# Optimization experiments

Hardware: AMD Instinct MI355X
Metric: run time of the kernel (lower is better)

Reference implementation:

```python
import jax, jax.numpy as jnp
import numpy as np

L, B, H, E, V = 64, 2048, 512, 50, 96
PAD = 0  # padding_idx of the char embedding


def setup_inputs() -> dict:
    key = jax.random.key(0)
    ks = jax.random.split(key, 10)
    s = 0.1  # param scale to keep gates in a sane range
    emb = jax.random.normal(ks[0], (V, E), jnp.float32) * s
    emb = emb.at[PAD].set(0.0)  # padding_idx row is zero
    return {
        "input_ids": jax.random.randint(ks[1], (L, B), 0, V),
        "h0": jax.random.normal(ks[2], (1, B, H), jnp.float32) * s,
        "c0": jax.random.normal(ks[3], (1, B, H), jnp.float32) * s,
        "emb": emb,
        "W_ih": jax.random.normal(ks[4], (4 * H, E), jnp.float32) * s,
        "W_hh": jax.random.normal(ks[5], (4 * H, H), jnp.float32) * s,
        "b_ih": jax.random.normal(ks[6], (4 * H,), jnp.float32) * s,
        "b_hh": jax.random.normal(ks[7], (4 * H,), jnp.float32) * s,
        "W_out": jax.random.normal(ks[8], (V, H), jnp.float32) * s,
        "b_out": jax.random.normal(ks[9], (V,), jnp.float32) * s,
    }


def reference(input_ids, h0, c0, emb, W_ih, W_hh, b_ih, b_hh, W_out, b_out):
    # Embedding lookup: (L, B, E)
    x = emb[input_ids]
    # Precompute input-side gate contributions for all steps: (L, B, 4H)
    x_gates = jnp.einsum('lbe,ge->lbg', x, W_ih) + b_ih + b_hh

    def step(carry, xg):
        h, c = carry  # (B, H) each
        gates = xg + h @ W_hh.T  # (B, 4H), PyTorch gate order i, f, g, o
        i, f, g, o = jnp.split(gates, 4, axis=-1)
        c_new = jax.nn.sigmoid(f) * c + jax.nn.sigmoid(i) * jnp.tanh(g)
        h_new = jax.nn.sigmoid(o) * jnp.tanh(c_new)
        return (h_new, c_new), h_new

    (hL, cL), hs = jax.lax.scan(step, (h0[0], c0[0]), x_gates)
    # Output projection on every step's hidden state: (L, B, V)
    scores = jnp.einsum('lbh,vh->lbv', hs, W_out) + b_out
    return scores, hL[None], cL[None]
```

## Files before the change

kernel.cpp:

```cpp
#include <hip/hip_runtime.h>
#include <stdint.h>

#define LSEQ 64
#define BATCH 2048
#define HID 512
#define NG 2048
#define KP 576
#define VOCAB 96
#define BH (BATCH*HID)

#define WLDS_OFF 0
#define RING_OFF 98304
#define HPK_OFF  147456
#define SMEM_TOT 155648

typedef unsigned short u16;
typedef __attribute__((ext_vector_type(8))) short short8;
typedef __attribute__((ext_vector_type(4))) float f32x4;

__device__ __forceinline__ u16 f2bf(float f) {
    union { float f; unsigned u; } v; v.f = f;
    return (u16)((v.u + 0x7FFFu + ((v.u >> 16) & 1u)) >> 16);
}
__device__ __forceinline__ float sig_(float x) { return 1.f / (1.f + __expf(-x)); }
__device__ __forceinline__ float th_(float x) {
    x = fminf(fmaxf(x, -30.f), 30.f);
    float e = __expf(2.f * x);
    return (e - 1.f) / (e + 1.f);
}
__device__ __forceinline__ void gld16(const void* g, void* l) {
    __builtin_amdgcn_global_load_lds(
        (const __attribute__((address_space(1))) unsigned int*)g,
        (__attribute__((address_space(3))) unsigned int*)l, 16, 0, 0);
}
#define WAITV(n) asm volatile("s_waitcnt vmcnt(" #n ")" ::: "memory")

__global__ void k_init(const float* __restrict__ h0, u16* __restrict__ hs0,
                       unsigned* __restrict__ flags) {
    int i = blockIdx.x * 256 + threadIdx.x;
    hs0[i] = f2bf(h0[i]);
    if (i < LSEQ * 256) flags[i] = 0;
}

__global__ void k_pack_w(const float* __restrict__ Wih, const float* __restrict__ Whh,
                         const float* __restrict__ bih, const float* __restrict__ bhh,
                         u16* __restrict__ Wp, float* __restrict__ bp) {
    int id = blockIdx.x * 256 + threadIdx.x;
    int n = id / 72, kc = id % 72;
    int j = n >> 2, q = n & 3;
    int src = q * HID + j;
    int k0 = kc * 8;
    unsigned pk[4];
#pragma unroll
    for (int t = 0; t < 4; ++t) {
        int k = k0 + 2 * t;
        float f0 = (k < 512) ? Whh[src * 512 + k] : ((k < 562) ? Wih[src * 50 + k - 512] : 0.f);
        float f1 = (k + 1 < 512) ? Whh[src * 512 + k + 1]
                                 : ((k + 1 < 562) ? Wih[src * 50 + k + 1 - 512] : 0.f);
        pk[t] = (unsigned)f2bf(f0) | ((unsigned)f2bf(f1) << 16);
    }
    *(uint4*)(Wp + (size_t)n * KP + k0) = make_uint4(pk[0], pk[1], pk[2], pk[3]);
    if (kc == 0) bp[n] = bih[src] + bhh[src];
}

__global__ void k_embed(const int* __restrict__ ids, const float* __restrict__ emb,
                        u16* __restrict__ xb) {
    int id = blockIdx.x * 256 + threadIdx.x;
    int row = id >> 3, kc = id & 7;
    int tok = ids[row];
    int k0 = kc * 8;
    unsigned pk[4];
#pragma unroll
    for (int t = 0; t < 4; ++t) {
        int k = k0 + 2 * t;
        unsigned lo = (k < 50) ? (unsigned)f2bf(emb[tok * 50 + k]) : 0u;
        unsigned hi = (k + 1 < 50) ? (unsigned)f2bf(emb[tok * 50 + k + 1]) : 0u;
        pk[t] = lo | (hi << 16);
    }
    *(uint4*)(xb + (size_t)row * 64 + k0) = make_uint4(pk[0], pk[1], pk[2], pk[3]);
}

__global__ void k_pack_wout(const float* __restrict__ Wo, u16* __restrict__ Wb) {
    int id = blockIdx.x * 256 + threadIdx.x;
    int k0 = id * 8;
    unsigned pk[4];
#pragma unroll
    for (int t = 0; t < 4; ++t)
        pk[t] = (unsigned)f2bf(Wo[k0 + 2 * t]) | ((unsigned)f2bf(Wo[k0 + 2 * t + 1]) << 16);
    *(uint4*)(Wb + k0) = make_uint4(pk[0], pk[1], pk[2], pk[3]);
}

__global__ __launch_bounds__(256, 1) void k_persist(
    const u16* __restrict__ xb, const u16* __restrict__ Wp,
    const float* __restrict__ bp, const float* __restrict__ c0,
    u16* __restrict__ hs, float* __restrict__ foutH, float* __restrict__ foutC,
    unsigned* __restrict__ flags)
{
    extern __shared__ char smem[];
    char* Wlds = smem + WLDS_OFF;
    char* ring = smem + RING_OFF;
    u16*  hpk  = (u16*)(smem + HPK_OFF);

    const int tid = threadIdx.x;
    const int lane = tid & 63;
    const int w = tid >> 6;
    const int wm = w >> 1, wn = w & 1;
    const int bm = blockIdx.x & 15, bn = blockIdx.x >> 4;
    const int m0 = bm * 128, n0 = bn * 128;
    const int rsub = lane >> 3;
    const int colsw = (((lane & 7) ^ rsub) << 3);
    const int bsub = lane & 15;
    const int usub = lane >> 4;

#pragma unroll
    for (int t = 0; t < 6; ++t)
#pragma unroll
        for (int it = 0; it < 4; ++it) {
            int wc = w * 4 + it;
            gld16(Wp + (size_t)(n0 + wc * 8 + rsub) * KP + (t + 2) * 64 + colsw,
                  Wlds + t * 16384 + wc * 1024);
        }

    short8 wreg[3][2][4];
#pragma unroll
    for (int t = 0; t < 3; ++t) {
        const int koff = (t == 0) ? 512 : (t - 1) * 64;
#pragma unroll
        for (int kk = 0; kk < 2; ++kk)
#pragma unroll
            for (int qm = 0; qm < 4; ++qm)
                wreg[t][kk][qm] = *(const short8*)(
                    Wp + (size_t)(n0 + wm * 64 + qm * 16 + bsub) * KP
                       + koff + kk * 32 + usub * 8);
    }

    float4 bb[4];
#pragma unroll
    for (int qm = 0; qm < 4; ++qm)
        bb[qm] = *(const float4*)(bp + n0 + wm * 64 + qm * 16 + usub * 4);
    float c[4][4];
#pragma unroll
    for (int qm = 0; qm < 4; ++qm)
#pragma unroll
        for (int qn = 0; qn < 4; ++qn)
            c[qm][qn] = c0[(size_t)(m0 + wn * 64 + qn * 16 + bsub) * HID
                           + (n0 >> 2) + wm * 16 + qm * 4 + usub];

    WAITV(0);
    __syncthreads();

#pragma unroll 1
    for (int l = 0; l < LSEQ; ++l) {
        const u16* hsrc = hs + (size_t)l * BH;

        {
            const u16* xs = xb + (size_t)l * BATCH * 64;
#pragma unroll
            for (int it = 0; it < 4; ++it) {
                int wc = w * 4 + it;
                gld16(xs + (size_t)(m0 + wc * 8 + rsub) * 64 + colsw, ring + wc * 1024);
            }
        }
        if (l > 0 && w == 0) {
            const unsigned* f = flags + (unsigned)(l - 1) * 256 + bm * 16;
            for (;;) {
                unsigned v = (lane < 16)
                    ? __hip_atomic_load(f + lane, __ATOMIC_RELAXED, __HIP_MEMORY_SCOPE_AGENT)
                    : 1u;
                if (__all(v != 0)) break;
                __builtin_amdgcn_s_sleep(2);
            }
        }
        __syncthreads();
        __builtin_amdgcn_sched_barrier(0);

#pragma unroll
        for (int it = 0; it < 4; ++it) {
            int wc = w * 4 + it;
            gld16(hsrc + (size_t)(m0 + wc * 8 + rsub) * HID + colsw,
                  ring + 16384 + wc * 1024);
        }

        f32x4 acc[4][4] = {};
#pragma unroll
        for (int i = 0; i < 9; ++i) {
            if (i > 0) {
                if (i < 8) WAITV(4); else WAITV(0);
                __builtin_amdgcn_s_barrier();
                __builtin_amdgcn_sched_barrier(0);
            }
            if (i + 2 <= 8) {
                char* dst = ring + ((i + 2) % 3) * 16384;
#pragma unroll
                for (int it = 0; it < 4; ++it) {
                    int wc = w * 4 + it;
                    gld16(hsrc + (size_t)(m0 + wc * 8 + rsub) * HID + (i + 1) * 64 + colsw,
                          dst + wc * 1024);
                }
            }
            const u16* Bs_ = (const u16*)(ring + (i % 3) * 16384);
#pragma unroll
            for (int kk = 0; kk < 2; ++kk) {
                short8 hv[4];
#pragma unroll
                for (int qn = 0; qn < 4; ++qn)
                    hv[qn] = *(const short8*)(Bs_ + (wn * 64 + qn * 16 + bsub) * 64
                                 + (((kk * 4 + usub) ^ (lane & 7)) << 3));
                short8 wf[4];
                if (i <= 2) {
#pragma unroll
                    for (int qm = 0; qm < 4; ++qm) wf[qm] = wreg[i][kk][qm];
                } else {
                    const u16* Ws_ = (const u16*)(Wlds + (i - 3) * 16384);
#pragma unroll
                    for (int qm = 0; qm < 4; ++qm)
                        wf[qm] = *(const short8*)(Ws_ + (wm * 64 + qm * 16 + bsub) * 64
                                     + (((kk * 4 + usub) ^ (lane & 7)) << 3));
                }
#pragma unroll
                for (int qm = 0; qm < 4; ++qm)
#pragma unroll
                    for (int qn = 0; qn < 4; ++qn)
                        acc[qm][qn] = __builtin_amdgcn_mfma_f32_16x16x32_bf16(
                            wf[qm], hv[qn], acc[qm][qn], 0, 0, 0);
            }
        }

        const bool last = (l == LSEQ - 1);
#pragma unroll
        for (int qm = 0; qm < 4; ++qm) {
            const float4 b4 = bb[qm];
            const int u_loc = wm * 16 + qm * 4 + usub;
#pragma unroll
            for (int qn = 0; qn < 4; ++qn) {
                const int b_loc = wn * 64 + qn * 16 + bsub;
                float gi = acc[qm][qn][0] + b4.x;
                float gf = acc[qm][qn][1] + b4.y;
                float gg = acc[qm][qn][2] + b4.z;
                float go = acc[qm][qn][3] + b4.w;
                float cn = sig_(gf) * c[qm][qn] + sig_(gi) * th_(gg);
                float hn = sig_(go) * th_(cn);
                c[qm][qn] = cn;
                hpk[b_loc * 32 + (u_loc ^ ((b_loc & 7) << 2))] = f2bf(hn);
                if (last) {
                    size_t ci = (size_t)(m0 + b_loc) * HID + (n0 >> 2) + u_loc;
                    foutH[ci] = hn; foutC[ci] = cn;
                }
            }
        }
        __syncthreads();

        {
            const int b = tid >> 1, hf = tid & 1;
            unsigned long long q[4];
#pragma unroll
            for (int g = 0; g < 4; ++g) {
                int G = hf * 4 + g;
                int gs = G ^ (b & 7);
                q[g] = *(const unsigned long long*)((const char*)hpk + b * 64 + gs * 8);
            }
            u16* dst = hs + (size_t)(l + 1) * BH + (size_t)(m0 + b) * HID
                       + (n0 >> 2) + hf * 16;
            *(uint4*)(dst)     = make_uint4((unsigned)q[0], (unsigned)(q[0] >> 32),
                                            (unsigned)q[1], (unsigned)(q[1] >> 32));
            *(uint4*)(dst + 8) = make_uint4((unsigned)q[2], (unsigned)(q[2] >> 32),
                                            (unsigned)q[3], (unsigned)(q[3] >> 32));
        }
        WAITV(0);
        __syncthreads();
        if (tid == 0)
            __hip_atomic_store(flags + (unsigned)l * 256 + bm * 16 + bn, 1u,
                               __ATOMIC_RELAXED, __HIP_MEMORY_SCOPE_AGENT);
    }
}

__global__ __launch_bounds__(256) void k_scores(
    const u16* __restrict__ hsall, const u16* __restrict__ Wb,
    const float* __restrict__ bo, float* __restrict__ out)
{
    __shared__ char smem[28672];
    u16* As = (u16*)smem;
    u16* Bs = (u16*)(smem + 16384);
    const int tid = threadIdx.x, lane = tid & 63, w = tid >> 6;
    const size_t m0 = (size_t)blockIdx.x * 128;
    const int colo = (lane & 7) * 8;
    const int rsub = lane >> 3;
    f32x4 acc[2][6] = {};

    for (int kt = 0; kt < 8; ++kt) {
#pragma unroll
        for (int it = 0; it < 4; ++it) {
            int wc = w * 4 + it;
            int r = wc * 8 + rsub;
            gld16(hsall + (m0 + r) * 512 + kt * 64 + colo, smem + wc * 1024);
        }
#pragma unroll
        for (int it = 0; it < 3; ++it) {
            int wc = w * 3 + it;
            int r = wc * 8 + rsub;
            gld16(Wb + (size_t)r * 512 + kt * 64 + colo, smem + 16384 + wc * 1024);
        }
        __syncthreads();
#pragma unroll
        for (int kk = 0; kk < 2; ++kk) {
            short8 av[2], bv[6];
#pragma unroll
            for (int i = 0; i < 2; ++i)
                av[i] = *(const short8*)(As + (w * 32 + i * 16 + (lane & 15)) * 64 + kk * 32 + (lane >> 4) * 8);
#pragma unroll
            for (int j = 0; j < 6; ++j)
                bv[j] = *(const short8*)(Bs + (j * 16 + (lane & 15)) * 64 + kk * 32 + (lane >> 4) * 8);
#pragma unroll
            for (int i = 0; i < 2; ++i)
#pragma unroll
                for (int j = 0; j < 6; ++j)
                    acc[i][j] = __builtin_amdgcn_mfma_f32_16x16x32_bf16(av[i], bv[j], acc[i][j], 0, 0, 0);
        }
        __syncthreads();
    }
#pragma unroll
    for (int i = 0; i < 2; ++i) {
        int ml = w * 32 + i * 16 + (lane >> 4) * 4;
#pragma unroll
        for (int j = 0; j < 6; ++j) {
            int v = j * 16 + (lane & 15);
            float bbv = bo[v];
#pragma unroll
            for (int r = 0; r < 4; ++r)
                out[(m0 + ml + r) * 96 + v] = acc[i][j][r] + bbv;
        }
    }
}

extern "C" void kernel_launch(void* const* d_in, const int* in_sizes, int n_in,
                              void* d_out, int out_size, void* d_ws, size_t ws_size,
                              hipStream_t stream) {
    const int*   ids  = (const int*)d_in[0];
    const float* h0   = (const float*)d_in[1];
    const float* c0   = (const float*)d_in[2];
    const float* emb  = (const float*)d_in[3];
    const float* Wih  = (const float*)d_in[4];
    const float* Whh  = (const float*)d_in[5];
    const float* bih  = (const float*)d_in[6];
    const float* bhh  = (const float*)d_in[7];
    const float* Wout = (const float*)d_in[8];
    const float* bout = (const float*)d_in[9];

    char* ws = (char*)d_ws;
    u16*      hs    = (u16*)ws;
    unsigned* flags = (unsigned*)(ws + 136314880);
    u16*      xb    = (u16*)(ws + 140509184);
    u16*      Wp    = (u16*)(ws + 157286400);
    float*    bp    = (float*)(ws + 159645696);
    u16*      Wb    = (u16*)(ws + 159653888);
    float*    out   = (float*)d_out;

    k_init<<<dim3(BH / 256), dim3(256), 0, stream>>>(h0, hs, flags);
    k_pack_w<<<dim3(NG * 72 / 256), dim3(256), 0, stream>>>(Wih, Whh, bih, bhh, Wp, bp);
    k_embed<<<dim3(LSEQ * BATCH * 8 / 256), dim3(256), 0, stream>>>(ids, emb, xb);
    k_pack_wout<<<dim3(VOCAB * HID / 8 / 256), dim3(256), 0, stream>>>(Wout, Wb);

    hipFuncSetAttribute((const void*)k_persist,
                        hipFuncAttributeMaxDynamicSharedMemorySize, SMEM_TOT);
    k_persist<<<dim3(256), dim3(256), SMEM_TOT, stream>>>(
        xb, Wp, bp, c0, hs, out + 12582912, out + 12582912 + BH, flags);

    k_scores<<<dim3(LSEQ * BATCH / 128), dim3(256), 0, stream>>>(hs + BH, Wb, bout, out);
}
```

Before: 577.2 us.

## Load h and x operands directly into registers, keep all W_hh slices in LDS

```diff
diff --git a/kernel.cpp b/kernel.cpp
--- a/kernel.cpp
+++ b/kernel.cpp
@@ -10,9 +10,8 @@
 #define BH (BATCH*HID)
 
 #define WLDS_OFF 0
-#define RING_OFF 98304
-#define HPK_OFF  147456
-#define SMEM_TOT 155648
+#define HPK_OFF  131072
+#define SMEM_TOT 139264
 
 typedef unsigned short u16;
 typedef __attribute__((ext_vector_type(8))) short short8;
@@ -98,7 +97,6 @@
 {
     extern __shared__ char smem[];
     char* Wlds = smem + WLDS_OFF;
-    char* ring = smem + RING_OFF;
     u16*  hpk  = (u16*)(smem + HPK_OFF);
 
     const int tid = threadIdx.x;
@@ -111,28 +109,25 @@
     const int colsw = (((lane & 7) ^ rsub) << 3);
     const int bsub = lane & 15;
     const int usub = lane >> 4;
-
-#pragma unroll
-    for (int t = 0; t < 6; ++t)
+    const int brow = m0 + wn * 64 + bsub;
+
+#pragma unroll
+    for (int t = 0; t < 8; ++t)
 #pragma unroll
         for (int it = 0; it < 4; ++it) {
             int wc = w * 4 + it;
-            gld16(Wp + (size_t)(n0 + wc * 8 + rsub) * KP + (t + 2) * 64 + colsw,
+            gld16(Wp + (size_t)(n0 + wc * 8 + rsub) * KP + t * 64 + colsw,
                   Wlds + t * 16384 + wc * 1024);
         }
 
-    short8 wreg[3][2][4];
-#pragma unroll
-    for (int t = 0; t < 3; ++t) {
-        const int koff = (t == 0) ? 512 : (t - 1) * 64;
-#pragma unroll
-        for (int kk = 0; kk < 2; ++kk)
-#pragma unroll
-            for (int qm = 0; qm < 4; ++qm)
-                wreg[t][kk][qm] = *(const short8*)(
-                    Wp + (size_t)(n0 + wm * 64 + qm * 16 + bsub) * KP
-                       + koff + kk * 32 + usub * 8);
-    }
+    short8 wrx[2][4];
+#pragma unroll
+    for (int kk = 0; kk < 2; ++kk)
+#pragma unroll
+        for (int qm = 0; qm < 4; ++qm)
+            wrx[kk][qm] = *(const short8*)(
+                Wp + (size_t)(n0 + wm * 64 + qm * 16 + bsub) * KP
+                   + 512 + kk * 32 + usub * 8);
 
     float4 bb[4];
 #pragma unroll
@@ -143,24 +138,26 @@
     for (int qm = 0; qm < 4; ++qm)
 #pragma unroll
         for (int qn = 0; qn < 4; ++qn)
-            c[qm][qn] = c0[(size_t)(m0 + wn * 64 + qn * 16 + bsub) * HID
+            c[qm][qn] = c0[(size_t)(brow + qn * 16) * HID
                            + (n0 >> 2) + wm * 16 + qm * 4 + usub];
 
     WAITV(0);
     __syncthreads();
+
+    short8 pA[8], pB[8];
 
 #pragma unroll 1
     for (int l = 0; l < LSEQ; ++l) {
         const u16* hsrc = hs + (size_t)l * BH;
-
-        {
-            const u16* xs = xb + (size_t)l * BATCH * 64;
-#pragma unroll
-            for (int it = 0; it < 4; ++it) {
-                int wc = w * 4 + it;
-                gld16(xs + (size_t)(m0 + wc * 8 + rsub) * 64 + colsw, ring + wc * 1024);
-            }
-        }
+        const u16* xsrc = xb + (size_t)l * BATCH * 64;
+
+#pragma unroll
+        for (int kk = 0; kk < 2; ++kk)
+#pragma unroll
+            for (int qn = 0; qn < 4; ++qn)
+                pA[kk * 4 + qn] = *(const short8*)(
+                    xsrc + (size_t)(brow + qn * 16) * 64 + kk * 32 + usub * 8);
+
         if (l > 0 && w == 0) {
             const unsigned* f = flags + (unsigned)(l - 1) * 256 + bm * 16;
             for (;;) {
@@ -175,43 +172,26 @@
         __builtin_amdgcn_sched_barrier(0);
 
 #pragma unroll
-        for (int it = 0; it < 4; ++it) {
-            int wc = w * 4 + it;
-            gld16(hsrc + (size_t)(m0 + wc * 8 + rsub) * HID + colsw,
-                  ring + 16384 + wc * 1024);
-        }
+        for (int kk = 0; kk < 2; ++kk)
+#pragma unroll
+            for (int qn = 0; qn < 4; ++qn)
+                pB[kk * 4 + qn] = *(const short8*)(
+                    hsrc + (size_t)(brow + qn * 16) * HID + kk * 32 + usub * 8);
 
         f32x4 acc[4][4] = {};
 #pragma unroll
         for (int i = 0; i < 9; ++i) {
-            if (i > 0) {
-                if (i < 8) WAITV(4); else WAITV(0);
-                __builtin_amdgcn_s_barrier();
-                __builtin_amdgcn_sched_barrier(0);
-            }
-            if (i + 2 <= 8) {
-                char* dst = ring + ((i + 2) % 3) * 16384;
-#pragma unroll
-                for (int it = 0; it < 4; ++it) {
-                    int wc = w * 4 + it;
-                    gld16(hsrc + (size_t)(m0 + wc * 8 + rsub) * HID + (i + 1) * 64 + colsw,
-                          dst + wc * 1024);
-                }
-            }
-            const u16* Bs_ = (const u16*)(ring + (i % 3) * 16384);
+            if (i < 8) WAITV(8); else WAITV(0);
+            __builtin_amdgcn_sched_barrier(0);
+            short8* cur = (i & 1) ? pB : pA;
 #pragma unroll
             for (int kk = 0; kk < 2; ++kk) {
-                short8 hv[4];
-#pragma unroll
-                for (int qn = 0; qn < 4; ++qn)
-                    hv[qn] = *(const short8*)(Bs_ + (wn * 64 + qn * 16 + bsub) * 64
-                                 + (((kk * 4 + usub) ^ (lane & 7)) << 3));
                 short8 wf[4];
-                if (i <= 2) {
-#pragma unroll
-                    for (int qm = 0; qm < 4; ++qm) wf[qm] = wreg[i][kk][qm];
+                if (i == 0) {
+#pragma unroll
+                    for (int qm = 0; qm < 4; ++qm) wf[qm] = wrx[kk][qm];
                 } else {
-                    const u16* Ws_ = (const u16*)(Wlds + (i - 3) * 16384);
+                    const u16* Ws_ = (const u16*)(Wlds + (i - 1) * 16384);
 #pragma unroll
                     for (int qm = 0; qm < 4; ++qm)
                         wf[qm] = *(const short8*)(Ws_ + (wm * 64 + qm * 16 + bsub) * 64
@@ -222,7 +202,17 @@
 #pragma unroll
                     for (int qn = 0; qn < 4; ++qn)
                         acc[qm][qn] = __builtin_amdgcn_mfma_f32_16x16x32_bf16(
-                            wf[qm], hv[qn], acc[qm][qn], 0, 0, 0);
+                            wf[qm], cur[kk * 4 + qn], acc[qm][qn], 0, 0, 0);
+            }
+            __builtin_amdgcn_sched_barrier(0);
+            if (i + 2 <= 8) {
+#pragma unroll
+                for (int kk = 0; kk < 2; ++kk)
+#pragma unroll
+                    for (int qn = 0; qn < 4; ++qn)
+                        cur[kk * 4 + qn] = *(const short8*)(
+                            hsrc + (size_t)(brow + qn * 16) * HID
+                                 + (i + 1) * 64 + kk * 32 + usub * 8);
             }
         }
 
```

Result: slower. 850.6 us (+47.4%).
